# Kernel optimization log

Measured on AMD Instinct MI355X. Metric: run time of the kernel, lower is better.

Reference implementation:

```python
import jax, jax.numpy as jnp
import numpy as np
from jax import lax

NDIMS = 3
NUM_SCALES = 3
WINDOW_SIZE = 9
POOL_K = 3


def box_filter(x, win):
    """Separable mean (box) filter, kernel=ones/win^3, same padding. x: [N,C,D,H,W]."""
    pad = win // 2
    for ax in range(NDIMS):
        kshape = [1, 1] + [1] * NDIMS
        kshape[2 + ax] = win
        k = jnp.ones(kshape, x.dtype) / win
        padding = [(pad, pad) if i == ax else (0, 0) for i in range(NDIMS)]
        x = lax.conv_general_dilated(x, k, window_strides=(1,) * NDIMS,
                                     padding=padding,
                                     dimension_numbers=('NCDHW', 'OIDHW', 'NCDHW'))
    return x


def avg_pool3d(x, k=POOL_K, stride=2):
    """avg_pool3d with count_include_pad=False."""
    pad = k // 2
    window = (1, 1, k, k, k)
    strides = (1, 1, stride, stride, stride)
    padding = ((0, 0), (0, 0), (pad, pad), (pad, pad), (pad, pad))
    s = lax.reduce_window(x, jnp.array(0, x.dtype), lax.add, window, strides, padding)
    cnt = lax.reduce_window(jnp.ones_like(x), jnp.array(0, x.dtype), lax.add,
                            window, strides, padding)
    return s / cnt


def single_scale_ncc(Ii, Ji, win):
    mu1 = box_filter(Ii, win)
    mu2 = box_filter(Ji, win)
    sigma1_sq = box_filter(Ii * Ii, win) - mu1 * mu1
    sigma2_sq = box_filter(Ji * Ji, win) - mu2 * mu2
    sigma12 = box_filter(Ii * Ji, win) - mu1 * mu2
    eps = jnp.finfo(sigma12.dtype).eps
    cc = sigma12 * sigma12 / jnp.maximum(sigma1_sq * sigma2_sq, eps)
    return -jnp.mean(cc)


def setup_inputs() -> dict:
    key = jax.random.key(0)
    k1, k2 = jax.random.split(key)
    shape = (2, 1, 160, 192, 160)
    I = jax.random.uniform(k1, shape, dtype=jnp.float32)
    J = jax.random.uniform(k2, shape, dtype=jnp.float32)
    return {"I": I, "J": J}


def reference(I, J):
    # Multi-scale NCC: losses at windows 9/7/5 on pyramid built by stride-2 avg pooling.
    total = jnp.zeros((), I.dtype)
    for i in range(NUM_SCALES):
        # SingleScaleNCC(pred=I, target=J): Ii=target, Ji=pred (symmetric metric)
        total = total + single_scale_ncc(J, I, WINDOW_SIZE - 2 * i) / NUM_SCALES
        if i < NUM_SCALES - 1:
            I = avg_pool3d(I)
            J = avg_pool3d(J)
    return total
```

## Files before the change

### kernel.cpp

```cpp
#include <hip/hip_runtime.h>

#define NCC_EPS 1.1920929e-07f

template<int WIN>
__global__ __launch_bounds__(256)
void ncc_pad3_kernel(const float* __restrict__ Pi, const float* __restrict__ Pj,
                     int Dp, int Hp, int Wp, int Dreal, int Wreal,
                     int tilesH, int tilesW, int chunksD, int chunkLen,
                     double* __restrict__ acc)
{
    constexpr int RAD  = WIN / 2;
    constexpr int TH = 16, TW = 16;
    constexpr int WROWS = TH + 2 * RAD;
    constexpr int PSTR = 68;
    constexpr int QSTR = 16;
    constexpr int HSTR = 68;
    constexpr int H4STR = 16;
    constexpr int OFF  = 4 - RAD;
    constexpr int NWT  = WROWS * 4;
    constexpr float invV = 1.0f / (float)(WIN * WIN * WIN);

    __shared__ __align__(16) float wb0123[2][WROWS * PSTR];
    __shared__ __align__(16) float wb4[2][WROWS * QSTR];
    __shared__ __align__(16) float hw0123[2][TH * HSTR];
    __shared__ __align__(16) float hw4[2][TH * H4STR];
    __shared__ float red[4];

    int bid = blockIdx.x;
    int tw = bid % tilesW; bid /= tilesW;
    int th = bid % tilesH; bid /= tilesH;
    int cd = bid % chunksD; bid /= chunksD;
    int b  = bid;

    const int h0 = th * TH, w0 = tw * TW;
    const int z0 = cd * chunkLen;
    const int z1 = min(z0 + chunkLen, Dreal);

    const size_t plane = (size_t)Hp * Wp;
    const float* Ib = Pi + (size_t)b * Dp * plane;
    const float* Jb = Pj + (size_t)b * Dp * plane;

    const int t  = threadIdx.x;
    const int hh = t >> 4, ww = t & 15;
    const bool valid = (w0 + ww) < Wreal;

    const int wsl  = (t >= NWT) ? 1 : 0;
    const bool wact = t < 2 * NWT;
    const int wt  = t - NWT * wsl;
    const int wr  = wt >> 2;
    const int wc4 = wt & 3;
    const size_t rowoff = (size_t)(h0 + wr) * Wp + (w0 + 4 * wc4);

    const bool hact = t < 128;
    const int hs = t >> 6;
    const int hc = t & 15;
    const int hg = (t >> 4) & 3;

    auto load_slice = [&](int zp, float (&fi)[12], float (&fj)[12]) {
        if (wact) {
            const float* rI = Ib + (size_t)zp * plane + rowoff;
            const float* rJ = Jb + (size_t)zp * plane + rowoff;
            float4 a0 = *reinterpret_cast<const float4*>(rI);
            float4 a1 = *reinterpret_cast<const float4*>(rI + 4);
            float4 a2 = *reinterpret_cast<const float4*>(rI + 8);
            float4 b0 = *reinterpret_cast<const float4*>(rJ);
            float4 b1 = *reinterpret_cast<const float4*>(rJ + 4);
            float4 b2 = *reinterpret_cast<const float4*>(rJ + 8);
            fi[0]=a0.x; fi[1]=a0.y; fi[2]=a0.z; fi[3]=a0.w;
            fi[4]=a1.x; fi[5]=a1.y; fi[6]=a1.z; fi[7]=a1.w;
            fi[8]=a2.x; fi[9]=a2.y; fi[10]=a2.z; fi[11]=a2.w;
            fj[0]=b0.x; fj[1]=b0.y; fj[2]=b0.z; fj[3]=b0.w;
            fj[4]=b1.x; fj[5]=b1.y; fj[6]=b1.z; fj[7]=b1.w;
            fj[8]=b2.x; fj[9]=b2.y; fj[10]=b2.z; fj[11]=b2.w;
        }
    };

    float ring[WIN][5];
    float rs[5];
    #pragma unroll
    for (int s = 0; s < WIN; ++s)
        #pragma unroll
        for (int c = 0; c < 5; ++c) ring[s][c] = 0.f;
    #pragma unroll
    for (int c = 0; c < 5; ++c) rs[c] = 0.f;

    float ccsum = 0.f;

    float fiC[12], fjC[12], fiN[12], fjN[12];
    const int zstart = z0 - RAD;
    const int zend   = z1 + RAD;
    load_slice(zstart + wsl + 4, fiC, fjC);

    for (int zb = zstart; zb < zend; zb += 2 * WIN) {
        #pragma unroll
        for (int i = 0; i < WIN; ++i) {
            const int z = zb + 2 * i;
            if (z < zend) {
                const bool haveB = (z + 1 < zend);
                const int zpn = min(z + wsl + 2 + 4, Dp - 1);
                load_slice(zpn, fiN, fjN);

                if (wact) {
                    float s0 = 0, s1 = 0, s2 = 0, s3 = 0, s4 = 0;
                    #pragma unroll
                    for (int k = 0; k < WIN; ++k) {
                        float a = fiC[OFF + k], bb = fjC[OFF + k];
                        s0 += a; s1 += bb;
                        s2 = fmaf(a, a, s2);
                        s3 = fmaf(bb, bb, s3);
                        s4 = fmaf(bb, a, s4);
                    }
                    float o0[4], o1[4], o2[4], o3[4], o4[4];
                    o0[0]=s0; o1[0]=s1; o2[0]=s2; o3[0]=s3; o4[0]=s4;
                    #pragma unroll
                    for (int m = 1; m < 4; ++m) {
                        float aL = fiC[OFF + m - 1],       bL = fjC[OFF + m - 1];
                        float aR = fiC[OFF + m - 1 + WIN], bR = fjC[OFF + m - 1 + WIN];
                        s0 += aR - aL;
                        s1 += bR - bL;
                        s2 = s2 + aR * aR - aL * aL;
                        s3 = s3 + bR * bR - bL * bL;
                        s4 = s4 + aR * bR - aL * bL;
                        o0[m]=s0; o1[m]=s1; o2[m]=s2; o3[m]=s3; o4[m]=s4;
                    }
                    float* wbW = &wb0123[wsl][0];
                    float* w4W = &wb4[wsl][0];
                    #pragma unroll
                    for (int m = 0; m < 4; ++m) {
                        *reinterpret_cast<float4*>(&wbW[wr * PSTR + 16 * wc4 + 4 * m]) =
                            make_float4(o0[m], o1[m], o2[m], o3[m]);
                    }
                    *reinterpret_cast<float4*>(&w4W[wr * QSTR + 4 * wc4]) =
                        make_float4(o4[0], o4[1], o4[2], o4[3]);
                }
                __builtin_amdgcn_sched_barrier(0);
                asm volatile("s_waitcnt lgkmcnt(0)");
                __builtin_amdgcn_s_barrier();
                __builtin_amdgcn_sched_barrier(0);
                if (hact) {
                    const float* wbS = &wb0123[hs][0];
                    const float* w4S = &wb4[hs][0];
                    float* hwS = &hw0123[hs][0];
                    float* h4S = &hw4[hs][0];
                    const int r0 = 4 * hg;
                    float4 a4 = make_float4(0.f, 0.f, 0.f, 0.f);
                    float a1 = 0.f;
                    float4 st4[3]; float st1[3];
                    #pragma unroll
                    for (int j = 0; j < WIN; ++j) {
                        float4 v = *reinterpret_cast<const float4*>(
                            &wbS[(r0 + j) * PSTR + 4 * hc]);
                        float w = w4S[(r0 + j) * QSTR + hc];
                        a4.x += v.x; a4.y += v.y; a4.z += v.z; a4.w += v.w;
                        a1 += w;
                        if (j < 3) { st4[j] = v; st1[j] = w; }
                    }
                    *reinterpret_cast<float4*>(&hwS[r0 * HSTR + 4 * hc]) = a4;
                    h4S[r0 * H4STR + hc] = a1;
                    #pragma unroll
                    for (int k = 1; k < 4; ++k) {
                        float4 vn = *reinterpret_cast<const float4*>(
                            &wbS[(r0 + WIN - 1 + k) * PSTR + 4 * hc]);
                        float wn = w4S[(r0 + WIN - 1 + k) * QSTR + hc];
                        a4.x += vn.x - st4[k - 1].x;
                        a4.y += vn.y - st4[k - 1].y;
                        a4.z += vn.z - st4[k - 1].z;
                        a4.w += vn.w - st4[k - 1].w;
                        a1 += wn - st1[k - 1];
                        *reinterpret_cast<float4*>(&hwS[(r0 + k) * HSTR + 4 * hc]) = a4;
                        h4S[(r0 + k) * H4STR + hc] = a1;
                    }
                }
                __builtin_amdgcn_sched_barrier(0);
                asm volatile("s_waitcnt lgkmcnt(0)");
                __builtin_amdgcn_s_barrier();
                __builtin_amdgcn_sched_barrier(0);
                {
                    float4 a4 = *reinterpret_cast<const float4*>(
                        &hw0123[0][hh * HSTR + 4 * ww]);
                    float nn4 = hw4[0][hh * H4STR + ww];
                    rs[0] += a4.x - ring[(2 * i) % WIN][0]; ring[(2 * i) % WIN][0] = a4.x;
                    rs[1] += a4.y - ring[(2 * i) % WIN][1]; ring[(2 * i) % WIN][1] = a4.y;
                    rs[2] += a4.z - ring[(2 * i) % WIN][2]; ring[(2 * i) % WIN][2] = a4.z;
                    rs[3] += a4.w - ring[(2 * i) % WIN][3]; ring[(2 * i) % WIN][3] = a4.w;
                    rs[4] += nn4  - ring[(2 * i) % WIN][4]; ring[(2 * i) % WIN][4] = nn4;
                    const int zo = z - RAD;
                    if (valid && zo >= z0) {
                        float muI = rs[0] * invV;
                        float muJ = rs[1] * invV;
                        float sII = rs[2] * invV - muI * muI;
                        float sJJ = rs[3] * invV - muJ * muJ;
                        float s12 = rs[4] * invV - muI * muJ;
                        float cc = (s12 * s12) / fmaxf(sII * sJJ, NCC_EPS);
                        ccsum += cc;
                    }
                }
                if (haveB) {
                    float4 a4 = *reinterpret_cast<const float4*>(
                        &hw0123[1][hh * HSTR + 4 * ww]);
                    float nn4 = hw4[1][hh * H4STR + ww];
                    rs[0] += a4.x - ring[(2 * i + 1) % WIN][0]; ring[(2 * i + 1) % WIN][0] = a4.x;
                    rs[1] += a4.y - ring[(2 * i + 1) % WIN][1]; ring[(2 * i + 1) % WIN][1] = a4.y;
                    rs[2] += a4.z - ring[(2 * i + 1) % WIN][2]; ring[(2 * i + 1) % WIN][2] = a4.z;
                    rs[3] += a4.w - ring[(2 * i + 1) % WIN][3]; ring[(2 * i + 1) % WIN][3] = a4.w;
                    rs[4] += nn4  - ring[(2 * i + 1) % WIN][4]; ring[(2 * i + 1) % WIN][4] = nn4;
                    const int zo = z + 1 - RAD;
                    if (valid && zo >= z0) {
                        float muI = rs[0] * invV;
                        float muJ = rs[1] * invV;
                        float sII = rs[2] * invV - muI * muI;
                        float sJJ = rs[3] * invV - muJ * muJ;
                        float s12 = rs[4] * invV - muI * muJ;
                        float cc = (s12 * s12) / fmaxf(sII * sJJ, NCC_EPS);
                        ccsum += cc;
                    }
                }
                #pragma unroll
                for (int e = 0; e < 12; ++e) { fiC[e] = fiN[e]; fjC[e] = fjN[e]; }
            }
        }
    }

    for (int off = 32; off > 0; off >>= 1)
        ccsum += __shfl_down(ccsum, off);
    const int wid = t >> 6, lane = t & 63;
    if (lane == 0) red[wid] = ccsum;
    __syncthreads();
    if (t == 0) {
        float s = red[0] + red[1] + red[2] + red[3];
        atomicAdd(acc, (double)s);
    }
}

template<int WIN>
__global__ __launch_bounds__(256)
void ncc_pad_kernel(const float* __restrict__ Pi, const float* __restrict__ Pj,
                    int Dp, int Hp, int Wp, int Dreal, int Wreal,
                    int tilesH, int tilesW, int chunksD, int chunkLen,
                    double* __restrict__ acc)
{
    constexpr int RAD  = WIN / 2;
    constexpr int TH = 16, TW = 16;
    constexpr int WROWS = TH + 2 * RAD;
    constexpr int PSTR = 68;
    constexpr int QSTR = 16;
    constexpr int OFF  = 4 - RAD;
    constexpr int NWT  = WROWS * 4;
    constexpr float invV = 1.0f / (float)(WIN * WIN * WIN);

    __shared__ __align__(16) float wb0123[2][WROWS * PSTR];
    __shared__ __align__(16) float wb4[2][WROWS * QSTR];
    __shared__ float red[4];

    int bid = blockIdx.x;
    int tw = bid % tilesW; bid /= tilesW;
    int th = bid % tilesH; bid /= tilesH;
    int cd = bid % chunksD; bid /= chunksD;
    int b  = bid;

    const int h0 = th * TH, w0 = tw * TW;
    const int z0 = cd * chunkLen;
    const int z1 = min(z0 + chunkLen, Dreal);

    const size_t plane = (size_t)Hp * Wp;
    const float* Ib = Pi + (size_t)b * Dp * plane;
    const float* Jb = Pj + (size_t)b * Dp * plane;

    const int t  = threadIdx.x;
    const int hh = t >> 4, ww = t & 15;
    const bool valid = (w0 + ww) < Wreal;

    const int wr  = t >> 2;
    const int wc4 = t & 3;
    const bool wact = t < NWT;
    const size_t rowoff = (size_t)(h0 + wr) * Wp + (w0 + 4 * wc4);

    auto load_slice = [&](int zp, float (&fi)[12], float (&fj)[12]) {
        if (wact) {
            const float* rI = Ib + (size_t)zp * plane + rowoff;
            const float* rJ = Jb + (size_t)zp * plane + rowoff;
            float4 a0 = *reinterpret_cast<const float4*>(rI);
            float4 a1 = *reinterpret_cast<const float4*>(rI + 4);
            float4 a2 = *reinterpret_cast<const float4*>(rI + 8);
            float4 b0 = *reinterpret_cast<const float4*>(rJ);
            float4 b1 = *reinterpret_cast<const float4*>(rJ + 4);
            float4 b2 = *reinterpret_cast<const float4*>(rJ + 8);
            fi[0]=a0.x; fi[1]=a0.y; fi[2]=a0.z; fi[3]=a0.w;
            fi[4]=a1.x; fi[5]=a1.y; fi[6]=a1.z; fi[7]=a1.w;
            fi[8]=a2.x; fi[9]=a2.y; fi[10]=a2.z; fi[11]=a2.w;
            fj[0]=b0.x; fj[1]=b0.y; fj[2]=b0.z; fj[3]=b0.w;
            fj[4]=b1.x; fj[5]=b1.y; fj[6]=b1.z; fj[7]=b1.w;
            fj[8]=b2.x; fj[9]=b2.y; fj[10]=b2.z; fj[11]=b2.w;
        }
    };

    float ring[WIN][5];
    float rs[5];
    #pragma unroll
    for (int s = 0; s < WIN; ++s)
        #pragma unroll
        for (int c = 0; c < 5; ++c) ring[s][c] = 0.f;
    #pragma unroll
    for (int c = 0; c < 5; ++c) rs[c] = 0.f;

    float ccsum = 0.f;

    float fiC[12], fjC[12], fiN[12], fjN[12];
    const int zend = z1 + RAD;
    load_slice(z0 - RAD + 4, fiC, fjC);

    for (int zb = z0 - RAD; zb < zend; zb += WIN) {
        #pragma unroll
        for (int ph = 0; ph < WIN; ++ph) {
            const int z = zb + ph;
            if (z < zend) {
                const int zpn = min(z + 5, Dp - 1);
                load_slice(zpn, fiN, fjN);

                const int par = (z + 4) & 1;
                float n0, n1, n2, n3, n4;
                if (wact) {
                    float s0 = 0, s1 = 0, s2 = 0, s3 = 0, s4 = 0;
                    #pragma unroll
                    for (int k = 0; k < WIN; ++k) {
                        float a = fiC[OFF + k], bb = fjC[OFF + k];
                        s0 += a; s1 += bb;
                        s2 = fmaf(a, a, s2);
                        s3 = fmaf(bb, bb, s3);
                        s4 = fmaf(a, bb, s4);
                    }
                    float o0[4], o1[4], o2[4], o3[4], o4[4];
                    o0[0]=s0; o1[0]=s1; o2[0]=s2; o3[0]=s3; o4[0]=s4;
                    #pragma unroll
                    for (int m = 1; m < 4; ++m) {
                        float aL = fiC[OFF + m - 1],       bL = fjC[OFF + m - 1];
                        float aR = fiC[OFF + m - 1 + WIN], bR = fjC[OFF + m - 1 + WIN];
                        s0 += aR - aL;
                        s1 += bR - bL;
                        s2 = s2 + aR * aR - aL * aL;
                        s3 = s3 + bR * bR - bL * bL;
                        s4 = s4 + aR * bR - aL * bL;
                        o0[m]=s0; o1[m]=s1; o2[m]=s2; o3[m]=s3; o4[m]=s4;
                    }
                    #pragma unroll
                    for (int m = 0; m < 4; ++m) {
                        *reinterpret_cast<float4*>(&wb0123[par][wr * PSTR + 16 * wc4 + 4 * m]) =
                            make_float4(o0[m], o1[m], o2[m], o3[m]);
                    }
                    *reinterpret_cast<float4*>(&wb4[par][wr * QSTR + 4 * wc4]) =
                        make_float4(o4[0], o4[1], o4[2], o4[3]);
                }
                __builtin_amdgcn_sched_barrier(0);
                asm volatile("s_waitcnt lgkmcnt(0)");
                __builtin_amdgcn_s_barrier();
                __builtin_amdgcn_sched_barrier(0);
                {
                    float4 a4 = make_float4(0.f, 0.f, 0.f, 0.f);
                    float nn4 = 0.f;
                    #pragma unroll
                    for (int dh = 0; dh < WIN; ++dh) {
                        float4 v = *reinterpret_cast<const float4*>(
                            &wb0123[par][(hh + dh) * PSTR + 4 * ww]);
                        a4.x += v.x; a4.y += v.y; a4.z += v.z; a4.w += v.w;
                        nn4 += wb4[par][(hh + dh) * QSTR + ww];
                    }
                    n0 = a4.x; n1 = a4.y; n2 = a4.z; n3 = a4.w; n4 = nn4;
                }
                rs[0] += n0 - ring[ph][0]; ring[ph][0] = n0;
                rs[1] += n1 - ring[ph][1]; ring[ph][1] = n1;
                rs[2] += n2 - ring[ph][2]; ring[ph][2] = n2;
                rs[3] += n3 - ring[ph][3]; ring[ph][3] = n3;
                rs[4] += n4 - ring[ph][4]; ring[ph][4] = n4;

                const int zo = z - RAD;
                if (valid && zo >= z0) {
                    float muI = rs[0] * invV;
                    float muJ = rs[1] * invV;
                    float sII = rs[2] * invV - muI * muI;
                    float sJJ = rs[3] * invV - muJ * muJ;
                    float s12 = rs[4] * invV - muI * muJ;
                    float cc = (s12 * s12) / fmaxf(sII * sJJ, NCC_EPS);
                    ccsum += cc;
                }
                #pragma unroll
                for (int e = 0; e < 12; ++e) { fiC[e] = fiN[e]; fjC[e] = fjN[e]; }
            }
        }
    }

    for (int off = 32; off > 0; off >>= 1)
        ccsum += __shfl_down(ccsum, off);
    const int wid = t >> 6, lane = t & 63;
    if (lane == 0) red[wid] = ccsum;
    __syncthreads();
    if (t == 0) {
        float s = red[0] + red[1] + red[2] + red[3];
        atomicAdd(acc, (double)s);
    }
}

__global__ void pad_kernel(const float* __restrict__ inA, const float* __restrict__ inB,
                           float* __restrict__ outA, float* __restrict__ outB,
                           int D, int H, int W, int Dp, int Hp, int Wp, int nchunks)
{
    int idx = blockIdx.x * 256 + threadIdx.x;
    if (idx >= 2 * nchunks) return;
    const bool isB = idx >= nchunks;
    int k = isB ? idx - nchunks : idx;
    const float* in = isB ? inB : inA;
    float* out = isB ? outB : outA;
    const int WC = Wp / 4;
    int wc = k % WC; int tmp = k / WC;
    int hp = tmp % Hp; tmp /= Hp;
    int zp = tmp % Dp; int b = tmp / Dp;
    int z = zp - 4, h = hp - 4, w0 = 4 * wc - 4;
    float4 v = make_float4(0.f, 0.f, 0.f, 0.f);
    if (z >= 0 && z < D && h >= 0 && h < H && w0 >= 0 && w0 + 4 <= W)
        v = *reinterpret_cast<const float4*>(in + ((size_t)(b * D + z) * H + h) * W + w0);
    *reinterpret_cast<float4*>(out + ((size_t)(b * Dp + zp) * Hp + hp) * Wp + 4 * wc) = v;
}

__global__ void pool_pad_kernel(const float* __restrict__ inA, const float* __restrict__ inB,
                                float* __restrict__ outA, float* __restrict__ outB,
                                int D, int H, int W, int iDp, int iHp, int iWp,
                                int oD, int oH, int oW, int oDp, int oHp, int oWp,
                                int total)
{
    int idx0 = blockIdx.x * 256 + threadIdx.x;
    if (idx0 >= 2 * total) return;
    const bool isB = idx0 >= total;
    int idx = isB ? idx0 - total : idx0;
    const float* in = isB ? inB : inA;
    float* out = isB ? outB : outA;

    int ow = idx % oW; int tmp = idx / oW;
    int oh = tmp % oH; tmp /= oH;
    int od = tmp % oD; int b = tmp / oD;

    const size_t ip = (size_t)iHp * iWp;
    const float* ib = in + (size_t)b * iDp * ip;
    float s = 0.f;
    #pragma unroll
    for (int dd = 0; dd < 3; ++dd)
        #pragma unroll
        for (int dh = 0; dh < 3; ++dh) {
            const float* r = ib + (size_t)(2 * od + 3 + dd) * ip
                                + (size_t)(2 * oh + 3 + dh) * iWp + (2 * ow + 3);
            s += r[0] + r[1] + r[2];
        }
    int dlo = max(2 * od - 1, 0), dhi = min(2 * od + 2, D);
    int hlo = max(2 * oh - 1, 0), hhi = min(2 * oh + 2, H);
    int wlo = max(2 * ow - 1, 0), whi = min(2 * ow + 2, W);
    int cnt = (dhi - dlo) * (hhi - hlo) * (whi - wlo);
    out[((size_t)(b * oDp + od + 4) * oHp + (oh + 4)) * oWp + (ow + 4)] = s / (float)cnt;
}

template<int WIN>
__global__ __launch_bounds__(256)
void ncc_scale_kernel(const float* __restrict__ I, const float* __restrict__ J,
                      int D, int H, int W,
                      int tilesH, int tilesW, int chunksD, int chunkLen,
                      double* __restrict__ acc)
{
    constexpr int RAD  = WIN / 2;
    constexpr int TH = 16, TW = 16;
    constexpr int WROWS = TH + 2 * RAD;
    constexpr int PSTR = 68;
    constexpr int QSTR = 16;
    constexpr int OFF  = 4 - RAD;
    constexpr int NWT  = WROWS * 4;
    constexpr float invV = 1.0f / (float)(WIN * WIN * WIN);

    __shared__ __align__(16) float wb0123[2][WROWS * PSTR];
    __shared__ __align__(16) float wb4[2][WROWS * QSTR];
    __shared__ float red[4];

    int bid = blockIdx.x;
    int tw = bid % tilesW; bid /= tilesW;
    int th = bid % tilesH; bid /= tilesH;
    int cd = bid % chunksD; bid /= chunksD;
    int b  = bid;

    const int h0 = th * TH, w0 = tw * TW;
    const int z0 = cd * chunkLen;
    const int z1 = min(z0 + chunkLen, D);

    const size_t plane = (size_t)H * W;
    const float* Ib = I + (size_t)b * D * plane;
    const float* Jb = J + (size_t)b * D * plane;

    const int t  = threadIdx.x;
    const int hh = t >> 4, ww = t & 15;
    const bool valid = (h0 + hh) < H && (w0 + ww) < W;

    const int wr  = t >> 2;
    const int wc4 = t & 3;
    const bool wact = t < NWT;
    const int wbase = w0 + 4 * wc4 - 4;
    const int wghr  = h0 + wr - RAD;

    auto load_slice = [&](int z, float (&fi)[12], float (&fj)[12]) {
        const bool zok = (z >= 0) && (z < D);
        if (zok && wact && wghr >= 0 && wghr < H) {
            const float* rowI = Ib + (size_t)z * plane + (size_t)wghr * W;
            const float* rowJ = Jb + (size_t)z * plane + (size_t)wghr * W;
            if (wbase >= 0 && wbase + 12 <= W) {
                float4 a0 = *reinterpret_cast<const float4*>(rowI + wbase);
                float4 a1 = *reinterpret_cast<const float4*>(rowI + wbase + 4);
                float4 a2 = *reinterpret_cast<const float4*>(rowI + wbase + 8);
                float4 b0 = *reinterpret_cast<const float4*>(rowJ + wbase);
                float4 b1 = *reinterpret_cast<const float4*>(rowJ + wbase + 4);
                float4 b2 = *reinterpret_cast<const float4*>(rowJ + wbase + 8);
                fi[0]=a0.x; fi[1]=a0.y; fi[2]=a0.z; fi[3]=a0.w;
                fi[4]=a1.x; fi[5]=a1.y; fi[6]=a1.z; fi[7]=a1.w;
                fi[8]=a2.x; fi[9]=a2.y; fi[10]=a2.z; fi[11]=a2.w;
                fj[0]=b0.x; fj[1]=b0.y; fj[2]=b0.z; fj[3]=b0.w;
                fj[4]=b1.x; fj[5]=b1.y; fj[6]=b1.z; fj[7]=b1.w;
                fj[8]=b2.x; fj[9]=b2.y; fj[10]=b2.z; fj[11]=b2.w;
            } else {
                #pragma unroll
                for (int e = 0; e < 12; ++e) {
                    int cg = wbase + e;
                    bool ok = (cg >= 0) && (cg < W);
                    fi[e] = ok ? rowI[cg] : 0.f;
                    fj[e] = ok ? rowJ[cg] : 0.f;
                }
            }
        } else {
            #pragma unroll
            for (int e = 0; e < 12; ++e) { fi[e] = 0.f; fj[e] = 0.f; }
        }
    };

    float ring[WIN][5];
    float rs[5];
    #pragma unroll
    for (int s = 0; s < WIN; ++s)
        #pragma unroll
        for (int c = 0; c < 5; ++c) ring[s][c] = 0.f;
    #pragma unroll
    for (int c = 0; c < 5; ++c) rs[c] = 0.f;

    float ccsum = 0.f;

    float fiC[12], fjC[12], fiN[12], fjN[12];
    const int zend = z1 + RAD;
    load_slice(z0 - RAD, fiC, fjC);

    for (int zb = z0 - RAD; zb < zend; zb += WIN) {
        #pragma unroll
        for (int ph = 0; ph < WIN; ++ph) {
            const int z = zb + ph;
            if (z < zend) {
                const bool zin = (z >= 0) && (z < D);
                load_slice((z + 1 < zend) ? z + 1 : -1, fiN, fjN);
                float n0 = 0, n1 = 0, n2 = 0, n3 = 0, n4 = 0;
                if (zin) {
                    const int par = (z + 64) & 1;
                    if (wact) {
                        float s0 = 0, s1 = 0, s2 = 0, s3 = 0, s4 = 0;
                        #pragma unroll
                        for (int k = 0; k < WIN; ++k) {
                            float a = fiC[OFF + k], bb = fjC[OFF + k];
                            s0 += a; s1 += bb;
                            s2 = fmaf(a, a, s2);
                            s3 = fmaf(bb, bb, s3);
                            s4 = fmaf(a, bb, s4);
                        }
                        float o0[4], o1[4], o2[4], o3[4], o4[4];
                        o0[0]=s0; o1[0]=s1; o2[0]=s2; o3[0]=s3; o4[0]=s4;
                        #pragma unroll
                        for (int m = 1; m < 4; ++m) {
                            float aL = fiC[OFF + m - 1],       bL = fjC[OFF + m - 1];
                            float aR = fiC[OFF + m - 1 + WIN], bR = fjC[OFF + m - 1 + WIN];
                            s0 += aR - aL;
                            s1 += bR - bL;
                            s2 = s2 + aR * aR - aL * aL;
                            s3 = s3 + bR * bR - bL * bL;
                            s4 = s4 + aR * bR - aL * bL;
                            o0[m]=s0; o1[m]=s1; o2[m]=s2; o3[m]=s3; o4[m]=s4;
                        }
                        #pragma unroll
                        for (int m = 0; m < 4; ++m) {
                            *reinterpret_cast<float4*>(&wb0123[par][wr * PSTR + 16 * wc4 + 4 * m]) =
                                make_float4(o0[m], o1[m], o2[m], o3[m]);
                        }
                        *reinterpret_cast<float4*>(&wb4[par][wr * QSTR + 4 * wc4]) =
                            make_float4(o4[0], o4[1], o4[2], o4[3]);
                    }
                    __syncthreads();
                    float4 a4 = make_float4(0.f, 0.f, 0.f, 0.f);
                    #pragma unroll
                    for (int dh = 0; dh < WIN; ++dh) {
                        float4 v = *reinterpret_cast<const float4*>(
                            &wb0123[par][(hh + dh) * PSTR + 4 * ww]);
                        a4.x += v.x; a4.y += v.y; a4.z += v.z; a4.w += v.w;
                        n4 += wb4[par][(hh + dh) * QSTR + ww];
                    }
                    n0 = a4.x; n1 = a4.y; n2 = a4.z; n3 = a4.w;
                }
                rs[0] += n0 - ring[ph][0]; ring[ph][0] = n0;
                rs[1] += n1 - ring[ph][1]; ring[ph][1] = n1;
                rs[2] += n2 - ring[ph][2]; ring[ph][2] = n2;
                rs[3] += n3 - ring[ph][3]; ring[ph][3] = n3;
                rs[4] += n4 - ring[ph][4]; ring[ph][4] = n4;

                const int zo = z - RAD;
                if (valid && zo >= z0) {
                    float muI = rs[0] * invV;
                    float muJ = rs[1] * invV;
                    float sII = rs[2] * invV - muI * muI;
                    float sJJ = rs[3] * invV - muJ * muJ;
                    float s12 = rs[4] * invV - muI * muJ;
                    float cc = (s12 * s12) / fmaxf(sII * sJJ, NCC_EPS);
                    ccsum += cc;
                }
                #pragma unroll
                for (int e = 0; e < 12; ++e) { fiC[e] = fiN[e]; fjC[e] = fjN[e]; }
            }
        }
    }

    for (int off = 32; off > 0; off >>= 1)
        ccsum += __shfl_down(ccsum, off);
    const int wid = t >> 6, lane = t & 63;
    if (lane == 0) red[wid] = ccsum;
    __syncthreads();
    if (t == 0) {
        float s = red[0] + red[1] + red[2] + red[3];
        atomicAdd(acc, (double)s);
    }
}

__global__ void pool_kernel2(const float* __restrict__ inA, const float* __restrict__ inB,
                             float* __restrict__ outA, float* __restrict__ outB,
                             int D, int H, int W, int oD, int oH, int oW, int total)
{
    int idx0 = blockIdx.x * 256 + threadIdx.x;
    if (idx0 >= 2 * total) return;
    const bool isB = idx0 >= total;
    int idx = isB ? idx0 - total : idx0;
    const float* in = isB ? inB : inA;
    float* out = isB ? outB : outA;

    int ow = idx % oW; int tmp = idx / oW;
    int oh = tmp % oH; tmp /= oH;
    int od = tmp % oD; int b = tmp / oD;

    int dlo = max(2 * od - 1, 0), dhi = min(2 * od + 2, D);
    int hlo = max(2 * oh - 1, 0), hhi = min(2 * oh + 2, H);
    int wlo = max(2 * ow - 1, 0), whi = min(2 * ow + 2, W);

    const float* ib = in + (size_t)b * D * H * W;
    float s = 0.f;
    for (int d = dlo; d < dhi; ++d)
        for (int h = hlo; h < hhi; ++h)
            for (int w = wlo; w < whi; ++w)
                s += ib[((size_t)d * H + h) * W + w];
    int cnt = (dhi - dlo) * (hhi - hlo) * (whi - wlo);
    out[idx] = s / (float)cnt;
}

__global__ void finalize_kernel(const double* __restrict__ acc, float* __restrict__ out)
{
    double m = acc[0] / 9830400.0 + acc[1] / 1228800.0 + acc[2] / 153600.0;
    out[0] = (float)(-m / 3.0);
}

extern "C" void kernel_launch(void* const* d_in, const int* in_sizes, int n_in,
                              void* d_out, int out_size, void* d_ws, size_t ws_size,
                              hipStream_t stream)
{
    const float* I0 = (const float*)d_in[0];
    const float* J0 = (const float*)d_in[1];
    float* out = (float*)d_out;

    char* ws = (char*)d_ws;
    double* acc = (double*)ws;
    hipMemsetAsync(acc, 0, 3 * sizeof(double), stream);

    const size_t P0SZ = (size_t)2 * 168 * 200 * 168;
    const size_t P1SZ = (size_t)2 * 88 * 104 * 88;
    const size_t P2SZ = (size_t)2 * 48 * 56 * 56;
    const size_t need_pad = 256 + (2 * P0SZ + 2 * P1SZ + 2 * P2SZ) * sizeof(float);

    if (ws_size >= need_pad) {
        float* P0I = (float*)(ws + 256);
        float* P0J = P0I + P0SZ;
        float* P1I = P0J + P0SZ;
        float* P1J = P1I + P1SZ;
        float* P2I = P1J + P1SZ;
        float* P2J = P2I + P2SZ;

        hipMemsetAsync(P1I, 0, (2 * P1SZ + 2 * P2SZ) * sizeof(float), stream);

        {
            int nchunks = (int)(P0SZ / 4);
            int blocks = (2 * nchunks + 255) / 256;
            pad_kernel<<<blocks, 256, 0, stream>>>(I0, J0, P0I, P0J,
                                                   160, 192, 160, 168, 200, 168, nchunks);
        }
        ncc_pad3_kernel<9><<<2 * 12 * 10 * 4, 256, 0, stream>>>(
            P0I, P0J, 168, 200, 168, 160, 160, 12, 10, 4, 40, acc + 0);
        {
            int total = 2 * 80 * 96 * 80;
            int blocks = (2 * total + 255) / 256;
            pool_pad_kernel<<<blocks, 256, 0, stream>>>(P0I, P0J, P1I, P1J,
                                                        160, 192, 160, 168, 200, 168,
                                                        80, 96, 80, 88, 104, 88, total);
        }
        ncc_pad_kernel<7><<<2 * 6 * 5 * 10, 256, 0, stream>>>(
            P1I, P1J, 88, 104, 88, 80, 80, 6, 5, 10, 8, acc + 1);
        {
            int total = 2 * 40 * 48 * 40;
            int blocks = (2 * total + 255) / 256;
            pool_pad_kernel<<<blocks, 256, 0, stream>>>(P1I, P1J, P2I, P2J,
                                                        80, 96, 80, 88, 104, 88,
                                                        40, 48, 40, 48, 56, 56, total);
        }
        ncc_pad_kernel<5><<<2 * 3 * 3 * 10, 256, 0, stream>>>(
            P2I, P2J, 48, 56, 56, 40, 40, 3, 3, 10, 4, acc + 2);
    } else {
        float* I1 = (float*)(ws + 256);
        float* J1 = I1 + (size_t)2 * 80 * 96 * 80;
        float* I2 = J1 + (size_t)2 * 80 * 96 * 80;
        float* J2 = I2 + (size_t)2 * 40 * 48 * 40;

        ncc_scale_kernel<9><<<2 * 12 * 10 * 6, 256, 0, stream>>>(
            I0, J0, 160, 192, 160, 12, 10, 6, 27, acc + 0);
        {
            int total = 2 * 80 * 96 * 80;
            int blocks = (2 * total + 255) / 256;
            pool_kernel2<<<blocks, 256, 0, stream>>>(I0, J0, I1, J1,
                                                     160, 192, 160, 80, 96, 80, total);
        }
        ncc_scale_kernel<7><<<2 * 6 * 5 * 10, 256, 0, stream>>>(
            I1, J1, 80, 96, 80, 6, 5, 10, 8, acc + 1);
        {
            int total = 2 * 40 * 48 * 40;
            int blocks = (2 * total + 255) / 256;
            pool_kernel2<<<blocks, 256, 0, stream>>>(I1, J1, I2, J2,
                                                     80, 96, 80, 40, 48, 40, total);
        }
        ncc_scale_kernel<5><<<2 * 3 * 3 * 10, 256, 0, stream>>>(
            I2, J2, 40, 48, 40, 3, 3, 10, 4, acc + 2);
    }

    finalize_kernel<<<1, 1, 0, stream>>>(acc, out);
}
```

Baseline: 168.9 us.

## Read interior tiles directly from input, pad only edge tiles into halo buffers

Replaces the full zero-padded copy of the level-0 volumes with a small edge-tile halo buffer, so interior tiles of the window-9 NCC kernel read the original input directly and only border tiles use pre-padded staging. Z-boundary padding is handled by zero-filling loads in the kernel. The first pooling step now reads the unpadded input with explicit bounds. This removes a large write and re-read of padded level-0 data, at the cost of branchier address setup, hardcoded geometry constants in the edge buffers, and unaligned interior reads.

```diff
diff --git a/kernel.cpp b/kernel.cpp
--- a/kernel.cpp
+++ b/kernel.cpp
@@ -4,10 +4,11 @@
 
 template<int WIN>
 __global__ __launch_bounds__(256)
-void ncc_pad3_kernel(const float* __restrict__ Pi, const float* __restrict__ Pj,
-                     int Dp, int Hp, int Wp, int Dreal, int Wreal,
-                     int tilesH, int tilesW, int chunksD, int chunkLen,
-                     double* __restrict__ acc)
+void ncc_uni_kernel(const float* __restrict__ I, const float* __restrict__ J,
+                    const float* __restrict__ EBI, const float* __restrict__ EBJ,
+                    int D, int H, int W,
+                    int tilesH, int tilesW, int chunksD, int chunkLen,
+                    double* __restrict__ acc)
 {
     constexpr int RAD  = WIN / 2;
     constexpr int TH = 16, TW = 16;
@@ -34,44 +35,68 @@
 
     const int h0 = th * TH, w0 = tw * TW;
     const int z0 = cd * chunkLen;
-    const int z1 = min(z0 + chunkLen, Dreal);
-
-    const size_t plane = (size_t)Hp * Wp;
-    const float* Ib = Pi + (size_t)b * Dp * plane;
-    const float* Jb = Pj + (size_t)b * Dp * plane;
+    const int z1 = min(z0 + chunkLen, D);
+
+    const int plane = H * W;
 
     const int t  = threadIdx.x;
     const int hh = t >> 4, ww = t & 15;
-    const bool valid = (w0 + ww) < Wreal;
+    const bool valid = (w0 + ww) < W;
 
     const int wsl  = (t >= NWT) ? 1 : 0;
     const bool wact = t < 2 * NWT;
     const int wt  = t - NWT * wsl;
     const int wr  = wt >> 2;
     const int wc4 = wt & 3;
-    const size_t rowoff = (size_t)(h0 + wr) * Wp + (w0 + 4 * wc4);
+
+    const bool isEdge = (th == 0) || (th == tilesH - 1) ||
+                        (tw == 0) || (tw == tilesW - 1);
+    const float *baseI, *baseJ;
+    int pstr;
+    if (isEdge) {
+        int e = (tw == 0) ? th
+              : (tw == tilesW - 1) ? 12 + th
+              : (th == 0) ? 24 + (tw - 1)
+              : 32 + (tw - 1);
+        size_t slot = (size_t)(e * 2 + b) * (size_t)(160 * 576);
+        int off = wr * 24 + 4 * wc4;
+        baseI = EBI + slot + off;
+        baseJ = EBJ + slot + off;
+        pstr = 576;
+    } else {
+        size_t off = (size_t)b * D * plane
+                   + (size_t)(h0 - 4 + wr) * W + (w0 - 4 + 4 * wc4);
+        baseI = I + off;
+        baseJ = J + off;
+        pstr = plane;
+    }
 
     const bool hact = t < 128;
     const int hs = t >> 6;
     const int hc = t & 15;
     const int hg = (t >> 4) & 3;
 
-    auto load_slice = [&](int zp, float (&fi)[12], float (&fj)[12]) {
+    auto load_slice = [&](int zu, float (&fi)[12], float (&fj)[12]) {
         if (wact) {
-            const float* rI = Ib + (size_t)zp * plane + rowoff;
-            const float* rJ = Jb + (size_t)zp * plane + rowoff;
-            float4 a0 = *reinterpret_cast<const float4*>(rI);
-            float4 a1 = *reinterpret_cast<const float4*>(rI + 4);
-            float4 a2 = *reinterpret_cast<const float4*>(rI + 8);
-            float4 b0 = *reinterpret_cast<const float4*>(rJ);
-            float4 b1 = *reinterpret_cast<const float4*>(rJ + 4);
-            float4 b2 = *reinterpret_cast<const float4*>(rJ + 8);
-            fi[0]=a0.x; fi[1]=a0.y; fi[2]=a0.z; fi[3]=a0.w;
-            fi[4]=a1.x; fi[5]=a1.y; fi[6]=a1.z; fi[7]=a1.w;
-            fi[8]=a2.x; fi[9]=a2.y; fi[10]=a2.z; fi[11]=a2.w;
-            fj[0]=b0.x; fj[1]=b0.y; fj[2]=b0.z; fj[3]=b0.w;
-            fj[4]=b1.x; fj[5]=b1.y; fj[6]=b1.z; fj[7]=b1.w;
-            fj[8]=b2.x; fj[9]=b2.y; fj[10]=b2.z; fj[11]=b2.w;
+            if (zu >= 0 && zu < D) {
+                const float* rI = baseI + (size_t)zu * pstr;
+                const float* rJ = baseJ + (size_t)zu * pstr;
+                float4 a0 = *reinterpret_cast<const float4*>(rI);
+                float4 a1 = *reinterpret_cast<const float4*>(rI + 4);
+                float4 a2 = *reinterpret_cast<const float4*>(rI + 8);
+                float4 b0 = *reinterpret_cast<const float4*>(rJ);
+                float4 b1 = *reinterpret_cast<const float4*>(rJ + 4);
+                float4 b2 = *reinterpret_cast<const float4*>(rJ + 8);
+                fi[0]=a0.x; fi[1]=a0.y; fi[2]=a0.z; fi[3]=a0.w;
+                fi[4]=a1.x; fi[5]=a1.y; fi[6]=a1.z; fi[7]=a1.w;
+                fi[8]=a2.x; fi[9]=a2.y; fi[10]=a2.z; fi[11]=a2.w;
+                fj[0]=b0.x; fj[1]=b0.y; fj[2]=b0.z; fj[3]=b0.w;
+                fj[4]=b1.x; fj[5]=b1.y; fj[6]=b1.z; fj[7]=b1.w;
+                fj[8]=b2.x; fj[9]=b2.y; fj[10]=b2.z; fj[11]=b2.w;
+            } else {
+                #pragma unroll
+                for (int e2 = 0; e2 < 12; ++e2) { fi[e2] = 0.f; fj[e2] = 0.f; }
+            }
         }
     };
 
@@ -89,7 +114,7 @@
     float fiC[12], fjC[12], fiN[12], fjN[12];
     const int zstart = z0 - RAD;
     const int zend   = z1 + RAD;
-    load_slice(zstart + wsl + 4, fiC, fjC);
+    load_slice(zstart + wsl, fiC, fjC);
 
     for (int zb = zstart; zb < zend; zb += 2 * WIN) {
         #pragma unroll
@@ -97,8 +122,7 @@
             const int z = zb + 2 * i;
             if (z < zend) {
                 const bool haveB = (z + 1 < zend);
-                const int zpn = min(z + wsl + 2 + 4, Dp - 1);
-                load_slice(zpn, fiN, fjN);
+                load_slice(z + wsl + 2, fiN, fjN);
 
                 if (wact) {
                     float s0 = 0, s1 = 0, s2 = 0, s3 = 0, s4 = 0;
@@ -216,7 +240,7 @@
                     }
                 }
                 #pragma unroll
-                for (int e = 0; e < 12; ++e) { fiC[e] = fiN[e]; fjC[e] = fjN[e]; }
+                for (int e2 = 0; e2 < 12; ++e2) { fiC[e2] = fiN[e2]; fjC[e2] = fjN[e2]; }
             }
         }
     }
@@ -230,6 +254,50 @@
         float s = red[0] + red[1] + red[2] + red[3];
         atomicAdd(acc, (double)s);
     }
+}
+
+__global__ void edgefill_kernel(const float* __restrict__ I, const float* __restrict__ J,
+                                float* __restrict__ EBI, float* __restrict__ EBJ,
+                                int D, int H, int W, int total)
+{
+    int idx = blockIdx.x * 256 + threadIdx.x;
+    if (idx >= 2 * total) return;
+    const bool isJ = idx >= total;
+    int k = isJ ? idx - total : idx;
+    const float* in = isJ ? J : I;
+    float* out = isJ ? EBJ : EBI;
+
+    int c = k % 6;  k /= 6;
+    int r = k % 24; k /= 24;
+    int z = k % 160; k /= 160;
+    int slot = k;
+    int e = slot >> 1, b = slot & 1;
+
+    int th, tw;
+    if (e < 12)      { th = e;      tw = 0; }
+    else if (e < 24) { th = e - 12; tw = 9; }
+    else if (e < 32) { th = 0;      tw = e - 24 + 1; }
+    else             { th = 11;     tw = e - 32 + 1; }
+
+    const int h = th * 16 - 4 + r;
+    const int w0c = tw * 16 - 4 + 4 * c;
+
+    float4 v = make_float4(0.f, 0.f, 0.f, 0.f);
+    if (h >= 0 && h < H) {
+        const float* row = in + ((size_t)(b * D + z) * H + h) * W;
+        if (w0c >= 0 && w0c + 4 <= W) {
+            v = *reinterpret_cast<const float4*>(row + w0c);
+        } else {
+            float tmp[4];
+            #pragma unroll
+            for (int q = 0; q < 4; ++q) {
+                int wq = w0c + q;
+                tmp[q] = (wq >= 0 && wq < W) ? row[wq] : 0.f;
+            }
+            v = make_float4(tmp[0], tmp[1], tmp[2], tmp[3]);
+        }
+    }
+    *reinterpret_cast<float4*>(&out[((size_t)slot * 160 + z) * 576 + r * 24 + 4 * c]) = v;
 }
 
 template<int WIN>
@@ -399,25 +467,34 @@
     }
 }
 
-__global__ void pad_kernel(const float* __restrict__ inA, const float* __restrict__ inB,
-                           float* __restrict__ outA, float* __restrict__ outB,
-                           int D, int H, int W, int Dp, int Hp, int Wp, int nchunks)
+__global__ void pool_b2p_kernel(const float* __restrict__ inA, const float* __restrict__ inB,
+                                float* __restrict__ outA, float* __restrict__ outB,
+                                int D, int H, int W, int oD, int oH, int oW,
+                                int oDp, int oHp, int oWp, int total)
 {
-    int idx = blockIdx.x * 256 + threadIdx.x;
-    if (idx >= 2 * nchunks) return;
-    const bool isB = idx >= nchunks;
-    int k = isB ? idx - nchunks : idx;
+    int idx0 = blockIdx.x * 256 + threadIdx.x;
+    if (idx0 >= 2 * total) return;
+    const bool isB = idx0 >= total;
+    int idx = isB ? idx0 - total : idx0;
     const float* in = isB ? inB : inA;
     float* out = isB ? outB : outA;
-    const int WC = Wp / 4;
-    int wc = k % WC; int tmp = k / WC;
-    int hp = tmp % Hp; tmp /= Hp;
-    int zp = tmp % Dp; int b = tmp / Dp;
-    int z = zp - 4, h = hp - 4, w0 = 4 * wc - 4;
-    float4 v = make_float4(0.f, 0.f, 0.f, 0.f);
-    if (z >= 0 && z < D && h >= 0 && h < H && w0 >= 0 && w0 + 4 <= W)
-        v = *reinterpret_cast<const float4*>(in + ((size_t)(b * D + z) * H + h) * W + w0);
-    *reinterpret_cast<float4*>(out + ((size_t)(b * Dp + zp) * Hp + hp) * Wp + 4 * wc) = v;
+
+    int ow = idx % oW; int tmp = idx / oW;
+    int oh = tmp % oH; tmp /= oH;
+    int od = tmp % oD; int b = tmp / oD;
+
+    int dlo = max(2 * od - 1, 0), dhi = min(2 * od + 2, D);
+    int hlo = max(2 * oh - 1, 0), hhi = min(2 * oh + 2, H);
+    int wlo = max(2 * ow - 1, 0), whi = min(2 * ow + 2, W);
+
+    const float* ib = in + (size_t)b * D * H * W;
+    float s = 0.f;
+    for (int d = dlo; d < dhi; ++d)
+        for (int h = hlo; h < hhi; ++h)
+            for (int w = wlo; w < whi; ++w)
+                s += ib[((size_t)d * H + h) * W + w];
+    int cnt = (dhi - dlo) * (hhi - hlo) * (whi - wlo);
+    out[((size_t)(b * oDp + od + 4) * oHp + (oh + 4)) * oWp + (ow + 4)] = s / (float)cnt;
 }
 
 __global__ void pool_pad_kernel(const float* __restrict__ inA, const float* __restrict__ inB,
@@ -679,15 +756,15 @@
     double* acc = (double*)ws;
     hipMemsetAsync(acc, 0, 3 * sizeof(double), stream);
 
-    const size_t P0SZ = (size_t)2 * 168 * 200 * 168;
+    const size_t EBSZ = (size_t)80 * 160 * 576;
     const size_t P1SZ = (size_t)2 * 88 * 104 * 88;
     const size_t P2SZ = (size_t)2 * 48 * 56 * 56;
-    const size_t need_pad = 256 + (2 * P0SZ + 2 * P1SZ + 2 * P2SZ) * sizeof(float);
-
-    if (ws_size >= need_pad) {
-        float* P0I = (float*)(ws + 256);
-        float* P0J = P0I + P0SZ;
-        float* P1I = P0J + P0SZ;
+    const size_t need = 256 + (2 * EBSZ + 2 * P1SZ + 2 * P2SZ) * sizeof(float);
+
+    if (ws_size >= need) {
+        float* EBI = (float*)(ws + 256);
+        float* EBJ = EBI + EBSZ;
+        float* P1I = EBJ + EBSZ;
         float* P1J = P1I + P1SZ;
         float* P2I = P1J + P1SZ;
         float* P2J = P2I + P2SZ;
@@ -695,19 +772,19 @@
         hipMemsetAsync(P1I, 0, (2 * P1SZ + 2 * P2SZ) * sizeof(float), stream);
 
         {
-            int nchunks = (int)(P0SZ / 4);
-            int blocks = (2 * nchunks + 255) / 256;
-            pad_kernel<<<blocks, 256, 0, stream>>>(I0, J0, P0I, P0J,
-                                                   160, 192, 160, 168, 200, 168, nchunks);
-        }
-        ncc_pad3_kernel<9><<<2 * 12 * 10 * 4, 256, 0, stream>>>(
-            P0I, P0J, 168, 200, 168, 160, 160, 12, 10, 4, 40, acc + 0);
+            int total = 80 * 160 * 24 * 6;
+            int blocks = (2 * total + 255) / 256;
+            edgefill_kernel<<<blocks, 256, 0, stream>>>(I0, J0, EBI, EBJ,
+                                                        160, 192, 160, total);
+        }
+        ncc_uni_kernel<9><<<2 * 12 * 10 * 4, 256, 0, stream>>>(
+            I0, J0, EBI, EBJ, 160, 192, 160, 12, 10, 4, 40, acc + 0);
         {
             int total = 2 * 80 * 96 * 80;
             int blocks = (2 * total + 255) / 256;
-            pool_pad_kernel<<<blocks, 256, 0, stream>>>(P0I, P0J, P1I, P1J,
-                                                        160, 192, 160, 168, 200, 168,
-                                                        80, 96, 80, 88, 104, 88, total);
+            pool_b2p_kernel<<<blocks, 256, 0, stream>>>(I0, J0, P1I, P1J,
+                                                        160, 192, 160, 80, 96, 80,
+                                                        88, 104, 88, total);
         }
         ncc_pad_kernel<7><<<2 * 6 * 5 * 10, 256, 0, stream>>>(
             P1I, P1J, 88, 104, 88, 80, 80, 6, 5, 10, 8, acc + 1);
```

After: 193.3 us. 1.14x slower.
